# Kernel tuning notes

Measured on AMD Instinct MI355X. Metric: run time of the kernel, lower is better.

The kernel has to match this reference:

```python
import jax, jax.numpy as jnp
import numpy as np

B, H, L, T, V = 256, 512, 3, 200, 100  # batch, hidden, lstm layers, decode steps (text_max_len-1), vocab


def setup_inputs() -> dict:
    key = jax.random.key(0)
    ks = jax.random.split(key, 12)
    s = 0.04  # ~1/sqrt(512), keeps gates in a sane range like trained weights
    return {
        "feat": jax.random.normal(ks[0], (B, H), jnp.float32),
        "visual_w": jax.random.normal(ks[1], (H, H), jnp.float32) * s,
        "visual_b": jax.random.normal(ks[2], (H,), jnp.float32) * s,
        "embed": jax.random.normal(ks[3], (V, H), jnp.float32),
        "w_ih": jax.random.normal(ks[4], (L, 4 * H, H), jnp.float32) * s,
        "w_hh": jax.random.normal(ks[5], (L, 4 * H, H), jnp.float32) * s,
        "b_ih": jax.random.normal(ks[6], (L, 4 * H), jnp.float32) * s,
        "b_hh": jax.random.normal(ks[7], (L, 4 * H), jnp.float32) * s,
        "proj_w1": jax.random.normal(ks[8], (2 * H, H), jnp.float32) * s,
        "proj_b1": jax.random.normal(ks[9], (2 * H,), jnp.float32) * s,
        "proj_w2": jax.random.normal(ks[10], (V, 2 * H), jnp.float32) * s,
        "proj_b2": jax.random.normal(ks[11], (V,), jnp.float32) * s,
        "start_idx": 1,  # tokenizer.char2idx[sos_token]
    }


def _lstm_stack_step(h, c, x, w_ih, w_hh, b_ih, b_hh):
    # h, c: [L, B, H]; x: [B, H]. PyTorch gate order: i, f, g, o.
    hs, cs = [], []
    for l in range(L):
        gates = x @ w_ih[l].T + b_ih[l] + h[l] @ w_hh[l].T + b_hh[l]  # [B, 4H]
        i, f, g, o = jnp.split(gates, 4, axis=-1)
        c_new = jax.nn.sigmoid(f) * c[l] + jax.nn.sigmoid(i) * jnp.tanh(g)
        h_new = jax.nn.sigmoid(o) * jnp.tanh(c_new)
        hs.append(h_new)
        cs.append(c_new)
        x = h_new  # inter-layer dropout is identity in eval mode
    return jnp.stack(hs), jnp.stack(cs), x


def reference(feat, visual_w, visual_b, embed, w_ih, w_hh, b_ih, b_hh,
              proj_w1, proj_b1, proj_w2, proj_b2, start_idx):
    # encoder feature -> visual_proj (applied once in forward, once more in _init_hidden)
    feat1 = feat @ visual_w.T + visual_b
    h0_layer = feat1 @ visual_w.T + visual_b           # same weights for every layer
    h0 = jnp.broadcast_to(h0_layer, (L, B, H))
    c0 = jnp.zeros((L, B, H), jnp.float32)
    x0 = jnp.broadcast_to(embed[start_idx], (B, H))    # embedded <sos>

    def step(carry, _):
        h, c, x = carry
        h, c, top = _lstm_stack_step(h, c, x, w_ih, w_hh, b_ih, b_hh)
        # next input is the top-layer output, detached (inp = out[-1:].detach())
        return (h, c, jax.lax.stop_gradient(top)), top

    (_, _, _), outs = jax.lax.scan(step, (h0, c0, x0), None, length=T)  # outs: [T, B, H]
    res = outs.transpose(1, 0, 2)                                       # [B, T, H]
    hmid = jax.nn.gelu(res @ proj_w1.T + proj_b1, approximate=False)    # [B, T, 2H]
    logits = hmid @ proj_w2.T + proj_b2                                  # [B, T, V]
    return logits.transpose(0, 2, 1)                                     # [B, V, T]
```

## Files before the change

### kernel.cpp

```cpp
#include <hip/hip_runtime.h>
#include <hip/hip_bf16.h>
#include <hip/hip_fp16.h>

#define NB 256
#define NH 512
#define NL 3
#define NT 200
#define NV 100
#define NVP 112
#define NG 2048
#define NK 1024
#define NS (NT * NL)

using f16x8 = __attribute__((ext_vector_type(8))) _Float16;
using f32x4 = __attribute__((ext_vector_type(4))) float;
using u32x4 = __attribute__((ext_vector_type(4))) unsigned int;

__device__ __forceinline__ float sigf(float x) { return 1.f / (1.f + __expf(-x)); }
__device__ __forceinline__ float tanhf_(float x) { return 2.f / (1.f + __expf(-2.f * x)) - 1.f; }

__global__ void k_probe(int* __restrict__ rowmap, int* __restrict__ colmap) {
  const int lane = threadIdx.x & 63;
  f16x8 a, b;
  const _Float16 idv = (_Float16)(float)(lane & 15);
  const _Float16 inv = (_Float16)(1.f / 32.f);
#pragma unroll
  for (int j = 0; j < 8; ++j) { a[j] = idv; b[j] = inv; }
  f32x4 d = {0.f, 0.f, 0.f, 0.f};
  d = __builtin_amdgcn_mfma_f32_16x16x32_f16(a, b, d, 0, 0, 0);
#pragma unroll
  for (int r = 0; r < 4; ++r) rowmap[lane * 4 + r] = (int)(d[r] + 0.5f);
#pragma unroll
  for (int j = 0; j < 8; ++j) { a[j] = inv; b[j] = idv; }
  f32x4 e = {0.f, 0.f, 0.f, 0.f};
  e = __builtin_amdgcn_mfma_f32_16x16x32_f16(a, b, e, 0, 0, 0);
#pragma unroll
  for (int r = 0; r < 4; ++r) colmap[lane * 4 + r] = (int)(e[r] + 0.5f);
}

__global__ void k_prep_w(const float* __restrict__ w_ih, const float* __restrict__ w_hh,
                         const float* __restrict__ b_ih, const float* __restrict__ b_hh,
                         _Float16* __restrict__ Wih, _Float16* __restrict__ Whh,
                         float* __restrict__ bias) {
  const int stride = gridDim.x * blockDim.x;
  const int tid0 = blockIdx.x * blockDim.x + threadIdx.x;
  for (int idx = tid0; idx < NL * NG * NH; idx += stride) {
    const int k = idx & (NH - 1);
    const int r = (idx >> 9) & (NG - 1);
    const int l = idx >> 20;
    const int hu = r >> 2, g = r & 3;
    const size_t soff = ((size_t)(l * NG + g * NH + hu)) * NH + k;
    Wih[idx] = (_Float16)w_ih[soff];
    Whh[idx] = (_Float16)w_hh[soff];
  }
  for (int idx = tid0; idx < NL * NG; idx += stride) {
    const int r = idx & (NG - 1);
    const int l = idx >> 11;
    const int hu = r >> 2, g = r & 3;
    const int srow = l * NG + g * NH + hu;
    bias[idx] = b_ih[srow] + b_hh[srow];
  }
}

__global__ void k_prep_misc(const float* __restrict__ embed, const int* __restrict__ start_idx,
                            const float* __restrict__ w1, const float* __restrict__ b1,
                            const float* __restrict__ w2, const float* __restrict__ b2,
                            _Float16* __restrict__ x0, _Float16* __restrict__ pw1, float* __restrict__ pb1,
                            _Float16* __restrict__ pw2, float* __restrict__ pb2, int* __restrict__ flags) {
  const int stride = gridDim.x * blockDim.x;
  const int tid0 = blockIdx.x * blockDim.x + threadIdx.x;
  for (int i = tid0; i < 256 * 16; i += stride) flags[i] = 0;
  const int st = start_idx[0];
  for (int i = tid0; i < NB * NH; i += stride)
    x0[i] = (_Float16)embed[(size_t)st * NH + (i & (NH - 1))];
  for (int i = tid0; i < 2 * NH * NH; i += stride)
    pw1[i] = (_Float16)w1[i];
  for (int i = tid0; i < NVP * NK; i += stride) {
    const int r = i >> 10;
    pw2[i] = (_Float16)((r < NV) ? w2[i] : 0.f);
  }
  for (int i = tid0; i < 2 * NH; i += stride) pb1[i] = b1[i];
  for (int i = tid0; i < NVP; i += stride) pb2[i] = (i < NV) ? b2[i] : 0.f;
}

__global__ void k_gemv512(const float* __restrict__ x, const float* __restrict__ w,
                          const float* __restrict__ bias, float* __restrict__ out) {
  const int b = blockIdx.x;
  __shared__ float xs[NH];
  for (int i = threadIdx.x; i < NH; i += 256) xs[i] = x[(size_t)b * NH + i];
  __syncthreads();
  const int wave = threadIdx.x >> 6, lane = threadIdx.x & 63;
  for (int j = wave; j < NH; j += 4) {
    const float* wr = w + (size_t)j * NH;
    float s = 0.f;
#pragma unroll
    for (int i = 0; i < 8; ++i) s += wr[lane + i * 64] * xs[lane + i * 64];
#pragma unroll
    for (int o = 32; o > 0; o >>= 1) s += __shfl_down(s, o);
    if (lane == 0) out[(size_t)b * NH + j] = s + bias[j];
  }
}

__global__ void k_gemv2_h0(const float* __restrict__ feat1, const float* __restrict__ w,
                           const float* __restrict__ bias, _Float16* __restrict__ h0b) {
  const int b = blockIdx.x;
  __shared__ float xs[NH];
  for (int i = threadIdx.x; i < NH; i += 256) xs[i] = feat1[(size_t)b * NH + i];
  __syncthreads();
  const int wave = threadIdx.x >> 6, lane = threadIdx.x & 63;
  for (int j = wave; j < NH; j += 4) {
    const float* wr = w + (size_t)j * NH;
    float s = 0.f;
#pragma unroll
    for (int i = 0; i < 8; ++i) s += wr[lane + i * 64] * xs[lane + i * 64];
#pragma unroll
    for (int o = 32; o > 0; o >>= 1) s += __shfl_down(s, o);
    if (lane == 0) h0b[(size_t)b * NH + j] = (_Float16)(s + bias[j]);
  }
}

__global__ __launch_bounds__(512, 2) void k_lstm(const _Float16* __restrict__ Wih,
                                                 const _Float16* __restrict__ Whh,
                                                 const float* __restrict__ bias,
                                                 _Float16* hx, const _Float16* __restrict__ h0b,
                                                 const _Float16* __restrict__ x0,
                                                 _Float16* __restrict__ outs,
                                                 const int* __restrict__ rowmap,
                                                 const int* __restrict__ colmap,
                                                 int* flags) {
  const int tid = threadIdx.x;
  const int lane = tid & 63;
  const int wave = tid >> 6;
  const int bid = blockIdx.x;
  const int jj = bid & 31;
  const int bm = bid >> 5;
  const int bn = (jj & 7) * 4 + (jj >> 3);
  const int gbase = bm * 32;
  const int wn = wave & 3;
  const int kh = wave >> 2;
  const int lr = lane & 15;
  const int lh = lane >> 4;
  const int nb0 = bn * 64 + wn * 16;
  __shared__ _Float16 Als[32][512];
  __shared__ float gl[2][32][68];
  __shared__ float pend[3][2][32][68];
  __shared__ _Float16 hout[32][16];

  int rm[4], cm[4];
#pragma unroll
  for (int r = 0; r < 4; ++r) {
    rm[r] = rowmap[lane * 4 + r];
    cm[r] = colmap[lane * 4 + r];
  }
  const int bl_ = tid >> 4;
  const int hu = tid & 15;
  float creg[NL] = {0.f, 0.f, 0.f};
  float bsv[NL][4];
#pragma unroll
  for (int l = 0; l < NL; ++l)
#pragma unroll
    for (int g = 0; g < 4; ++g) bsv[l][g] = bias[l * NG + (bn * 16 + hu) * 4 + g];

  f16x8 wx[8], wh[8], areg[16];

#define PREFETCH(LX, LZ)                                                          \
  do {                                                                            \
    const _Float16* wbx = Wih + ((size_t)((LX) * NG + nb0 + lr)) * NH + kh * 256 + lh * 8; \
    const _Float16* wbh = Whh + ((size_t)((LZ) * NG + nb0 + lr)) * NH + kh * 256 + lh * 8; \
    _Pragma("unroll") for (int k_ = 0; k_ < 8; ++k_) {                            \
      wx[k_] = *(const f16x8*)(wbx + k_ * 32);                                    \
      wh[k_] = *(const f16x8*)(wbh + k_ * 32);                                    \
    }                                                                             \
  } while (0)

#define LOAD_AREG()                                                               \
  do {                                                                            \
    _Pragma("unroll") for (int kk = 0; kk < 8; ++kk) {                            \
      const int c_ = kh * 32 + kk * 4 + lh;                                       \
      areg[kk] = *(const f16x8*)&Als[lr][(c_ ^ (lr & 7)) * 8];                    \
      areg[8 + kk] = *(const f16x8*)&Als[16 + lr][(c_ ^ (lr & 7)) * 8];           \
    }                                                                             \
  } while (0)

#define STAGE_A(SRC, VOLQ)                                                        \
  do {                                                                            \
    _Pragma("unroll") for (int c = 0; c < 4; ++c) {                               \
      const int i_ = tid + c * 512;                                               \
      const int rr = i_ >> 6, cc = i_ & 63;                                       \
      u32x4 v_ = *(const VOLQ u32x4*)((SRC) + (size_t)(bm * 32 + rr) * NH + cc * 8); \
      *(u32x4*)&Als[rr][(cc ^ (rr & 7)) * 8] = v_;                                \
    }                                                                             \
  } while (0)

  STAGE_A(h0b, );
  __syncthreads();
  LOAD_AREG();
#pragma unroll 1
  for (int lp = 0; lp < 3; ++lp) {
    const _Float16* wbh = Whh + ((size_t)(lp * NG + nb0 + lr)) * NH + kh * 256 + lh * 8;
    f16x8 wt[8];
#pragma unroll
    for (int k_ = 0; k_ < 8; ++k_) wt[k_] = *(const f16x8*)(wbh + k_ * 32);
    f32x4 a0 = {0.f, 0.f, 0.f, 0.f}, a1 = {0.f, 0.f, 0.f, 0.f};
#pragma unroll
    for (int kk = 0; kk < 8; ++kk) {
      a0 = __builtin_amdgcn_mfma_f32_16x16x32_f16(areg[kk], wt[kk], a0, 0, 0, 0);
      a1 = __builtin_amdgcn_mfma_f32_16x16x32_f16(areg[8 + kk], wt[kk], a1, 0, 0, 0);
    }
#pragma unroll
    for (int r = 0; r < 4; ++r) {
      pend[lp][kh][rm[r]][wn * 16 + cm[r]] = a0[r];
      pend[lp][kh][16 + rm[r]][wn * 16 + cm[r]] = a1[r];
    }
  }
  PREFETCH(0, 2);
  __syncthreads();
  STAGE_A(x0, );
  __syncthreads();

#pragma unroll 1
  for (int t = 0; t < NT; ++t) {
#pragma unroll
    for (int l = 0; l < NL; ++l) {
      const int s = t * 3 + l;
      LOAD_AREG();
      {
        f32x4 a0 = {0.f, 0.f, 0.f, 0.f}, a1 = {0.f, 0.f, 0.f, 0.f};
#pragma unroll
        for (int kk = 0; kk < 8; ++kk) {
          a0 = __builtin_amdgcn_mfma_f32_16x16x32_f16(areg[kk], wx[kk], a0, 0, 0, 0);
          a1 = __builtin_amdgcn_mfma_f32_16x16x32_f16(areg[8 + kk], wx[kk], a1, 0, 0, 0);
        }
#pragma unroll
        for (int r = 0; r < 4; ++r) {
          gl[kh][rm[r]][wn * 16 + cm[r]] = a0[r];
          gl[kh][16 + rm[r]][wn * 16 + cm[r]] = a1[r];
        }
      }
      __syncthreads();
      {
        const f32x4 gx0 = *(const f32x4*)&gl[0][bl_][hu * 4];
        const f32x4 gx1 = *(const f32x4*)&gl[1][bl_][hu * 4];
        const f32x4 gh0 = *(const f32x4*)&pend[l][0][bl_][hu * 4];
        const f32x4 gh1 = *(const f32x4*)&pend[l][1][bl_][hu * 4];
        const float gi = gx0[0] + gx1[0] + gh0[0] + gh1[0] + bsv[l][0];
        const float gf = gx0[1] + gx1[1] + gh0[1] + gh1[1] + bsv[l][1];
        const float gg = gx0[2] + gx1[2] + gh0[2] + gh1[2] + bsv[l][2];
        const float go = gx0[3] + gx1[3] + gh0[3] + gh1[3] + bsv[l][3];
        const float cn = sigf(gf) * creg[l] + sigf(gi) * tanhf_(gg);
        const float hn = sigf(go) * tanhf_(cn);
        creg[l] = cn;
        hout[bl_][hu] = (_Float16)hn;
      }
      __syncthreads();
      if (wave == 0) {
        const int row = lane >> 1, half = lane & 1;
        _Float16* dst = hx + (size_t)(s & 1) * NB * NH + (size_t)(bm * 32 + row) * NH + bn * 16 + half * 8;
        u32x4 v = *(const u32x4*)&hout[row][half * 8];
        *(volatile u32x4*)dst = v;
      }
      if (s >= 1 && s <= NS - 3) {
        const int l2 = (l + 2) % 3;
        f32x4 a0 = {0.f, 0.f, 0.f, 0.f}, a1 = {0.f, 0.f, 0.f, 0.f};
#pragma unroll
        for (int kk = 0; kk < 8; ++kk) {
          a0 = __builtin_amdgcn_mfma_f32_16x16x32_f16(areg[kk], wh[kk], a0, 0, 0, 0);
          a1 = __builtin_amdgcn_mfma_f32_16x16x32_f16(areg[8 + kk], wh[kk], a1, 0, 0, 0);
        }
#pragma unroll
        for (int r = 0; r < 4; ++r) {
          pend[l2][kh][rm[r]][wn * 16 + cm[r]] = a0[r];
          pend[l2][kh][16 + rm[r]][wn * 16 + cm[r]] = a1[r];
        }
      }
      if (wave == 0) {
        asm volatile("s_waitcnt vmcnt(0)" ::: "memory");
        if (lane == 0) *(volatile int*)&flags[(gbase + jj) * 16] = s + 1;
      }
      if (wave == 1 && l == 2) {
        const int row = lane >> 1, half = lane & 1;
        _Float16* dst = outs + ((size_t)t * NB + bm * 32 + row) * NH + bn * 16 + half * 8;
        *(u32x4*)dst = *(const u32x4*)&hout[row][half * 8];
      }
      if (s < NS - 1) {
        PREFETCH((l + 1) % 3, l);
        if (lane < 32) {
          const volatile int* fp = (const volatile int*)&flags[(gbase + lane) * 16];
          while (*fp < s + 1) __builtin_amdgcn_s_sleep(1);
        }
        STAGE_A(hx + (size_t)(s & 1) * NB * NH, volatile);
        __syncthreads();
      }
    }
  }
#undef STAGE_A
#undef LOAD_AREG
#undef PREFETCH
}

__global__ __launch_bounds__(256) void k_proj(const _Float16* __restrict__ outs, const _Float16* __restrict__ pw1,
                                              const float* __restrict__ pb1, const _Float16* __restrict__ pw2,
                                              const float* __restrict__ pb2,
                                              const int* __restrict__ rowmap, const int* __restrict__ colmap,
                                              float* __restrict__ out) {
  const int tid = threadIdx.x;
  const int lane = tid & 63;
  const int wave = tid >> 6;
  const int lr = lane & 15;
  const int lh = lane >> 4;
  const int mbase = blockIdx.x * 16;
  __shared__ _Float16 hm[16][NK + 8];
  int rm[4], cm[4];
#pragma unroll
  for (int r = 0; r < 4; ++r) {
    rm[r] = rowmap[lane * 4 + r];
    cm[r] = colmap[lane * 4 + r];
  }
  const int mrow = mbase + lr;
  const _Float16* ap = outs + ((size_t)(mrow % NT) * NB + (mrow / NT)) * NH + lh * 8;
  for (int nf = 0; nf < 16; ++nf) {
    const int n0 = wave * 256 + nf * 16;
    f32x4 acc = {0.f, 0.f, 0.f, 0.f};
    const _Float16* bp = pw1 + (size_t)(n0 + lr) * NH + lh * 8;
#pragma unroll 4
    for (int kk = 0; kk < 16; ++kk) {
      f16x8 a = *(const f16x8*)(ap + kk * 32);
      f16x8 b = *(const f16x8*)(bp + kk * 32);
      acc = __builtin_amdgcn_mfma_f32_16x16x32_f16(a, b, acc, 0, 0, 0);
    }
#pragma unroll
    for (int r = 0; r < 4; ++r) {
      const float v = acc[r] + pb1[n0 + cm[r]];
      const float gv = 0.5f * v * (1.f + erff(v * 0.70710678118654752f));
      hm[rm[r]][n0 + cm[r]] = (_Float16)gv;
    }
  }
  __syncthreads();
  for (int nf = wave; nf < 7; nf += 4) {
    const int n0 = nf * 16;
    f32x4 acc = {0.f, 0.f, 0.f, 0.f};
    const _Float16* bp = pw2 + (size_t)(n0 + lr) * NK + lh * 8;
#pragma unroll 4
    for (int kk = 0; kk < 32; ++kk) {
      f16x8 a = *(const f16x8*)(&hm[lr][kk * 32 + lh * 8]);
      f16x8 b = *(const f16x8*)(bp + kk * 32);
      acc = __builtin_amdgcn_mfma_f32_16x16x32_f16(a, b, acc, 0, 0, 0);
    }
#pragma unroll
    for (int r = 0; r < 4; ++r) {
      const int v = n0 + cm[r];
      if (v < NV) {
        const int m = mbase + rm[r];
        out[((size_t)(m / NT) * NV + v) * NT + (m % NT)] = acc[r] + pb2[v];
      }
    }
  }
}

extern "C" void kernel_launch(void* const* d_in, const int* in_sizes, int n_in,
                              void* d_out, int out_size, void* d_ws, size_t ws_size,
                              hipStream_t stream) {
  const float* feat = (const float*)d_in[0];
  const float* visual_w = (const float*)d_in[1];
  const float* visual_b = (const float*)d_in[2];
  const float* embed = (const float*)d_in[3];
  const float* w_ih = (const float*)d_in[4];
  const float* w_hh = (const float*)d_in[5];
  const float* b_ih = (const float*)d_in[6];
  const float* b_hh = (const float*)d_in[7];
  const float* proj_w1 = (const float*)d_in[8];
  const float* proj_b1 = (const float*)d_in[9];
  const float* proj_w2 = (const float*)d_in[10];
  const float* proj_b2 = (const float*)d_in[11];
  const int* start_idx = (const int*)d_in[12];
  float* out = (float*)d_out;

  char* ws = (char*)d_ws;
  size_t off = 0;
  auto alloc = [&](size_t bytes) -> void* {
    void* p = ws + off;
    off += (bytes + 255) & ~(size_t)255;
    return p;
  };
  _Float16* Wih = (_Float16*)alloc((size_t)NL * NG * NH * 2);
  _Float16* Whh = (_Float16*)alloc((size_t)NL * NG * NH * 2);
  float* bias = (float*)alloc((size_t)NL * NG * 4);
  _Float16* hx = (_Float16*)alloc((size_t)2 * NB * NH * 2);
  _Float16* h0b = (_Float16*)alloc((size_t)NB * NH * 2);
  _Float16* x0 = (_Float16*)alloc((size_t)NB * NH * 2);
  _Float16* outsb = (_Float16*)alloc((size_t)NT * NB * NH * 2);
  float* feat1 = (float*)alloc((size_t)NB * NH * 4);
  _Float16* pw1 = (_Float16*)alloc((size_t)2 * NH * NH * 2);
  _Float16* pw2 = (_Float16*)alloc((size_t)NVP * NK * 2);
  float* pb1 = (float*)alloc((size_t)2 * NH * 4);
  float* pb2 = (float*)alloc((size_t)NVP * 4);
  int* flags = (int*)alloc(256 * 16 * 4);
  int* rowmap = (int*)alloc(256 * 4);
  int* colmap = (int*)alloc(256 * 4);
  if (off > ws_size) return;

  k_probe<<<dim3(1), dim3(64), 0, stream>>>(rowmap, colmap);
  k_prep_w<<<dim3(2048), dim3(256), 0, stream>>>(w_ih, w_hh, b_ih, b_hh, Wih, Whh, bias);
  k_prep_misc<<<dim3(1024), dim3(256), 0, stream>>>(embed, start_idx, proj_w1, proj_b1, proj_w2, proj_b2,
                                                    x0, pw1, pb1, pw2, pb2, flags);
  k_gemv512<<<dim3(NB), dim3(256), 0, stream>>>(feat, visual_w, visual_b, feat1);
  k_gemv2_h0<<<dim3(NB), dim3(256), 0, stream>>>(feat1, visual_w, visual_b, h0b);
  k_lstm<<<dim3(256), dim3(512), 0, stream>>>(Wih, Whh, bias, hx, h0b, x0, outsb, rowmap, colmap, flags);
  k_proj<<<dim3(3200), dim3(256), 0, stream>>>(outsb, pw1, pb1, pw2, pb2, rowmap, colmap, out);
}
```

Before: 4.791 ms.

## Repartition persistent LSTM blocks to 16-row batch groups with full-K waves

Each block of the persistent LSTM kernel now covers 16 batch rows and 128 gate columns, in groups of 16 blocks, instead of 32 rows and 64 columns in groups of 32 blocks. Each wave now does the full K=512 reduction itself, so the cross-wave partial-sum buffers and the extra LDS reads in the gate stage go away. This also shrinks each flag barrier from 32 blocks to 16, which should cut synchronisation latency on every step. The recurrent Whh weights are no longer prefetched into registers but loaded from global memory inside the MFMA loop, which may add load latency on the critical path; the host launch grid must also match the new mapping.

Result: slower. 8.648 ms (+80.5%).

```diff
diff --git a/kernel.cpp b/kernel.cpp
--- a/kernel.cpp
+++ b/kernel.cpp
@@ -132,19 +132,16 @@
   const int lane = tid & 63;
   const int wave = tid >> 6;
   const int bid = blockIdx.x;
-  const int jj = bid & 31;
-  const int bm = bid >> 5;
-  const int bn = (jj & 7) * 4 + (jj >> 3);
-  const int gbase = bm * 32;
-  const int wn = wave & 3;
-  const int kh = wave >> 2;
+  const int jj = bid & 15;
+  const int gm = bid >> 4;
+  const int gbase = gm * 16;
   const int lr = lane & 15;
   const int lh = lane >> 4;
-  const int nb0 = bn * 64 + wn * 16;
-  __shared__ _Float16 Als[32][512];
-  __shared__ float gl[2][32][68];
-  __shared__ float pend[3][2][32][68];
-  __shared__ _Float16 hout[32][16];
+  const int nb0 = jj * 128 + wave * 16;
+  __shared__ _Float16 Als[16][512];
+  __shared__ float gl[16][132];
+  __shared__ float pend[3][16][132];
+  __shared__ _Float16 hout[16][32];
 
   int rm[4], cm[4];
 #pragma unroll
@@ -152,42 +149,36 @@
     rm[r] = rowmap[lane * 4 + r];
     cm[r] = colmap[lane * 4 + r];
   }
-  const int bl_ = tid >> 4;
-  const int hu = tid & 15;
+  const int row_ = tid >> 5;
+  const int huL = tid & 31;
   float creg[NL] = {0.f, 0.f, 0.f};
   float bsv[NL][4];
 #pragma unroll
   for (int l = 0; l < NL; ++l)
 #pragma unroll
-    for (int g = 0; g < 4; ++g) bsv[l][g] = bias[l * NG + (bn * 16 + hu) * 4 + g];
-
-  f16x8 wx[8], wh[8], areg[16];
-
-#define PREFETCH(LX, LZ)                                                          \
+    for (int g = 0; g < 4; ++g) bsv[l][g] = bias[l * NG + (jj * 32 + huL) * 4 + g];
+
+  f16x8 wx[16], areg[16];
+
+#define PREFETCH(LX)                                                              \
   do {                                                                            \
-    const _Float16* wbx = Wih + ((size_t)((LX) * NG + nb0 + lr)) * NH + kh * 256 + lh * 8; \
-    const _Float16* wbh = Whh + ((size_t)((LZ) * NG + nb0 + lr)) * NH + kh * 256 + lh * 8; \
-    _Pragma("unroll") for (int k_ = 0; k_ < 8; ++k_) {                            \
-      wx[k_] = *(const f16x8*)(wbx + k_ * 32);                                    \
-      wh[k_] = *(const f16x8*)(wbh + k_ * 32);                                    \
-    }                                                                             \
+    const _Float16* wbx = Wih + ((size_t)((LX) * NG + nb0 + lr)) * NH + lh * 8;   \
+    _Pragma("unroll") for (int k_ = 0; k_ < 16; ++k_)                             \
+        wx[k_] = *(const f16x8*)(wbx + k_ * 32);                                  \
   } while (0)
 
 #define LOAD_AREG()                                                               \
   do {                                                                            \
-    _Pragma("unroll") for (int kk = 0; kk < 8; ++kk) {                            \
-      const int c_ = kh * 32 + kk * 4 + lh;                                       \
-      areg[kk] = *(const f16x8*)&Als[lr][(c_ ^ (lr & 7)) * 8];                    \
-      areg[8 + kk] = *(const f16x8*)&Als[16 + lr][(c_ ^ (lr & 7)) * 8];           \
-    }                                                                             \
+    _Pragma("unroll") for (int kk = 0; kk < 16; ++kk)                             \
+      areg[kk] = *(const f16x8*)&Als[lr][(((kk) * 4 + lh) ^ (lr & 7)) * 8];       \
   } while (0)
 
 #define STAGE_A(SRC, VOLQ)                                                        \
   do {                                                                            \
-    _Pragma("unroll") for (int c = 0; c < 4; ++c) {                               \
+    _Pragma("unroll") for (int c = 0; c < 2; ++c) {                               \
       const int i_ = tid + c * 512;                                               \
       const int rr = i_ >> 6, cc = i_ & 63;                                       \
-      u32x4 v_ = *(const VOLQ u32x4*)((SRC) + (size_t)(bm * 32 + rr) * NH + cc * 8); \
+      u32x4 v_ = *(const VOLQ u32x4*)((SRC) + (size_t)(gm * 16 + rr) * NH + cc * 8); \
       *(u32x4*)&Als[rr][(cc ^ (rr & 7)) * 8] = v_;                                \
     }                                                                             \
   } while (0)
@@ -197,23 +188,18 @@
   LOAD_AREG();
 #pragma unroll 1
   for (int lp = 0; lp < 3; ++lp) {
-    const _Float16* wbh = Whh + ((size_t)(lp * NG + nb0 + lr)) * NH + kh * 256 + lh * 8;
-    f16x8 wt[8];
-#pragma unroll
-    for (int k_ = 0; k_ < 8; ++k_) wt[k_] = *(const f16x8*)(wbh + k_ * 32);
-    f32x4 a0 = {0.f, 0.f, 0.f, 0.f}, a1 = {0.f, 0.f, 0.f, 0.f};
+    const _Float16* wbh = Whh + ((size_t)(lp * NG + nb0 + lr)) * NH + lh * 8;
+    f32x4 aA = {0.f, 0.f, 0.f, 0.f}, aB = {0.f, 0.f, 0.f, 0.f};
 #pragma unroll
     for (int kk = 0; kk < 8; ++kk) {
-      a0 = __builtin_amdgcn_mfma_f32_16x16x32_f16(areg[kk], wt[kk], a0, 0, 0, 0);
-      a1 = __builtin_amdgcn_mfma_f32_16x16x32_f16(areg[8 + kk], wt[kk], a1, 0, 0, 0);
-    }
-#pragma unroll
-    for (int r = 0; r < 4; ++r) {
-      pend[lp][kh][rm[r]][wn * 16 + cm[r]] = a0[r];
-      pend[lp][kh][16 + rm[r]][wn * 16 + cm[r]] = a1[r];
-    }
-  }
-  PREFETCH(0, 2);
+      aA = __builtin_amdgcn_mfma_f32_16x16x32_f16(areg[kk], *(const f16x8*)(wbh + kk * 32), aA, 0, 0, 0);
+      aB = __builtin_amdgcn_mfma_f32_16x16x32_f16(areg[8 + kk], *(const f16x8*)(wbh + (8 + kk) * 32), aB, 0, 0, 0);
+    }
+#pragma unroll
+    for (int r = 0; r < 4; ++r)
+      pend[lp][rm[r]][wave * 16 + cm[r]] = aA[r] + aB[r];
+  }
+  PREFETCH(0);
   __syncthreads();
   STAGE_A(x0, );
   __syncthreads();
@@ -225,66 +211,61 @@
       const int s = t * 3 + l;
       LOAD_AREG();
       {
-        f32x4 a0 = {0.f, 0.f, 0.f, 0.f}, a1 = {0.f, 0.f, 0.f, 0.f};
+        f32x4 aA = {0.f, 0.f, 0.f, 0.f}, aB = {0.f, 0.f, 0.f, 0.f};
 #pragma unroll
         for (int kk = 0; kk < 8; ++kk) {
-          a0 = __builtin_amdgcn_mfma_f32_16x16x32_f16(areg[kk], wx[kk], a0, 0, 0, 0);
-          a1 = __builtin_amdgcn_mfma_f32_16x16x32_f16(areg[8 + kk], wx[kk], a1, 0, 0, 0);
+          aA = __builtin_amdgcn_mfma_f32_16x16x32_f16(areg[kk], wx[kk], aA, 0, 0, 0);
+          aB = __builtin_amdgcn_mfma_f32_16x16x32_f16(areg[8 + kk], wx[8 + kk], aB, 0, 0, 0);
         }
 #pragma unroll
-        for (int r = 0; r < 4; ++r) {
-          gl[kh][rm[r]][wn * 16 + cm[r]] = a0[r];
-          gl[kh][16 + rm[r]][wn * 16 + cm[r]] = a1[r];
-        }
+        for (int r = 0; r < 4; ++r)
+          gl[rm[r]][wave * 16 + cm[r]] = aA[r] + aB[r];
       }
       __syncthreads();
       {
-        const f32x4 gx0 = *(const f32x4*)&gl[0][bl_][hu * 4];
-        const f32x4 gx1 = *(const f32x4*)&gl[1][bl_][hu * 4];
-        const f32x4 gh0 = *(const f32x4*)&pend[l][0][bl_][hu * 4];
-        const f32x4 gh1 = *(const f32x4*)&pend[l][1][bl_][hu * 4];
-        const float gi = gx0[0] + gx1[0] + gh0[0] + gh1[0] + bsv[l][0];
-        const float gf = gx0[1] + gx1[1] + gh0[1] + gh1[1] + bsv[l][1];
-        const float gg = gx0[2] + gx1[2] + gh0[2] + gh1[2] + bsv[l][2];
-        const float go = gx0[3] + gx1[3] + gh0[3] + gh1[3] + bsv[l][3];
+        const f32x4 gx = *(const f32x4*)&gl[row_][huL * 4];
+        const f32x4 gh = *(const f32x4*)&pend[l][row_][huL * 4];
+        const float gi = gx[0] + gh[0] + bsv[l][0];
+        const float gf = gx[1] + gh[1] + bsv[l][1];
+        const float gg = gx[2] + gh[2] + bsv[l][2];
+        const float go = gx[3] + gh[3] + bsv[l][3];
         const float cn = sigf(gf) * creg[l] + sigf(gi) * tanhf_(gg);
         const float hn = sigf(go) * tanhf_(cn);
         creg[l] = cn;
-        hout[bl_][hu] = (_Float16)hn;
+        hout[row_][huL] = (_Float16)hn;
       }
       __syncthreads();
       if (wave == 0) {
-        const int row = lane >> 1, half = lane & 1;
-        _Float16* dst = hx + (size_t)(s & 1) * NB * NH + (size_t)(bm * 32 + row) * NH + bn * 16 + half * 8;
-        u32x4 v = *(const u32x4*)&hout[row][half * 8];
+        const int row = lane >> 2, q = lane & 3;
+        _Float16* dst = hx + (size_t)(s & 1) * NB * NH + (size_t)(gm * 16 + row) * NH + jj * 32 + q * 8;
+        u32x4 v = *(const u32x4*)&hout[row][q * 8];
         *(volatile u32x4*)dst = v;
       }
       if (s >= 1 && s <= NS - 3) {
         const int l2 = (l + 2) % 3;
-        f32x4 a0 = {0.f, 0.f, 0.f, 0.f}, a1 = {0.f, 0.f, 0.f, 0.f};
+        const _Float16* wbh = Whh + ((size_t)(l2 * NG + nb0 + lr)) * NH + lh * 8;
+        f32x4 aA = {0.f, 0.f, 0.f, 0.f}, aB = {0.f, 0.f, 0.f, 0.f};
 #pragma unroll
         for (int kk = 0; kk < 8; ++kk) {
-          a0 = __builtin_amdgcn_mfma_f32_16x16x32_f16(areg[kk], wh[kk], a0, 0, 0, 0);
-          a1 = __builtin_amdgcn_mfma_f32_16x16x32_f16(areg[8 + kk], wh[kk], a1, 0, 0, 0);
+          aA = __builtin_amdgcn_mfma_f32_16x16x32_f16(areg[kk], *(const f16x8*)(wbh + kk * 32), aA, 0, 0, 0);
+          aB = __builtin_amdgcn_mfma_f32_16x16x32_f16(areg[8 + kk], *(const f16x8*)(wbh + (8 + kk) * 32), aB, 0, 0, 0);
         }
 #pragma unroll
-        for (int r = 0; r < 4; ++r) {
-          pend[l2][kh][rm[r]][wn * 16 + cm[r]] = a0[r];
-          pend[l2][kh][16 + rm[r]][wn * 16 + cm[r]] = a1[r];
-        }
+        for (int r = 0; r < 4; ++r)
+          pend[l2][rm[r]][wave * 16 + cm[r]] = aA[r] + aB[r];
       }
       if (wave == 0) {
         asm volatile("s_waitcnt vmcnt(0)" ::: "memory");
         if (lane == 0) *(volatile int*)&flags[(gbase + jj) * 16] = s + 1;
       }
       if (wave == 1 && l == 2) {
-        const int row = lane >> 1, half = lane & 1;
-        _Float16* dst = outs + ((size_t)t * NB + bm * 32 + row) * NH + bn * 16 + half * 8;
-        *(u32x4*)dst = *(const u32x4*)&hout[row][half * 8];
+        const int row = lane >> 2, q = lane & 3;
+        _Float16* dst = outs + ((size_t)t * NB + gm * 16 + row) * NH + jj * 32 + q * 8;
+        *(u32x4*)dst = *(const u32x4*)&hout[row][q * 8];
       }
       if (s < NS - 1) {
-        PREFETCH((l + 1) % 3, l);
-        if (lane < 32) {
+        PREFETCH((l + 1) % 3);
+        if (lane < 16) {
           const volatile int* fp = (const volatile int*)&flags[(gbase + lane) * 16];
           while (*fp < s + 1) __builtin_amdgcn_s_sleep(1);
         }
```

## Merge setup kernels and retile projection to 32-row blocks with register-held A

Applied to the files above, without the earlier changes.

Fuses the probe and two weight-preparation kernels into one setup launch, removing two kernel launches. The projection kernel now handles 32 output rows per block: each wave keeps its 16x512 activation slice in registers and loops over half of the hidden columns, using two independent MFMA accumulator chains. This halves the number of blocks and the repeated loads of the first projection weights, at the cost of more registers and more shared memory per block, which may lower occupancy.

New measurement: 4.578 ms. 4.5% less time.

```diff
diff --git a/kernel.cpp b/kernel.cpp
--- a/kernel.cpp
+++ b/kernel.cpp
@@ -19,31 +19,36 @@
 __device__ __forceinline__ float sigf(float x) { return 1.f / (1.f + __expf(-x)); }
 __device__ __forceinline__ float tanhf_(float x) { return 2.f / (1.f + __expf(-2.f * x)) - 1.f; }
 
-__global__ void k_probe(int* __restrict__ rowmap, int* __restrict__ colmap) {
-  const int lane = threadIdx.x & 63;
-  f16x8 a, b;
-  const _Float16 idv = (_Float16)(float)(lane & 15);
-  const _Float16 inv = (_Float16)(1.f / 32.f);
-#pragma unroll
-  for (int j = 0; j < 8; ++j) { a[j] = idv; b[j] = inv; }
-  f32x4 d = {0.f, 0.f, 0.f, 0.f};
-  d = __builtin_amdgcn_mfma_f32_16x16x32_f16(a, b, d, 0, 0, 0);
-#pragma unroll
-  for (int r = 0; r < 4; ++r) rowmap[lane * 4 + r] = (int)(d[r] + 0.5f);
-#pragma unroll
-  for (int j = 0; j < 8; ++j) { a[j] = inv; b[j] = idv; }
-  f32x4 e = {0.f, 0.f, 0.f, 0.f};
-  e = __builtin_amdgcn_mfma_f32_16x16x32_f16(a, b, e, 0, 0, 0);
-#pragma unroll
-  for (int r = 0; r < 4; ++r) colmap[lane * 4 + r] = (int)(e[r] + 0.5f);
-}
-
-__global__ void k_prep_w(const float* __restrict__ w_ih, const float* __restrict__ w_hh,
-                         const float* __restrict__ b_ih, const float* __restrict__ b_hh,
-                         _Float16* __restrict__ Wih, _Float16* __restrict__ Whh,
-                         float* __restrict__ bias) {
+__global__ void k_setup(const float* __restrict__ w_ih, const float* __restrict__ w_hh,
+                        const float* __restrict__ b_ih, const float* __restrict__ b_hh,
+                        const float* __restrict__ embed, const int* __restrict__ start_idx,
+                        const float* __restrict__ w1, const float* __restrict__ b1,
+                        const float* __restrict__ w2, const float* __restrict__ b2,
+                        _Float16* __restrict__ Wih, _Float16* __restrict__ Whh,
+                        float* __restrict__ bias, _Float16* __restrict__ x0,
+                        _Float16* __restrict__ pw1, float* __restrict__ pb1,
+                        _Float16* __restrict__ pw2, float* __restrict__ pb2,
+                        int* __restrict__ flags, int* __restrict__ rowmap, int* __restrict__ colmap) {
   const int stride = gridDim.x * blockDim.x;
   const int tid0 = blockIdx.x * blockDim.x + threadIdx.x;
+  if (blockIdx.x == 0 && threadIdx.x < 64) {
+    const int lane = threadIdx.x & 63;
+    f16x8 a, b;
+    const _Float16 idv = (_Float16)(float)(lane & 15);
+    const _Float16 inv = (_Float16)(1.f / 32.f);
+#pragma unroll
+    for (int j = 0; j < 8; ++j) { a[j] = idv; b[j] = inv; }
+    f32x4 d = {0.f, 0.f, 0.f, 0.f};
+    d = __builtin_amdgcn_mfma_f32_16x16x32_f16(a, b, d, 0, 0, 0);
+#pragma unroll
+    for (int r = 0; r < 4; ++r) rowmap[lane * 4 + r] = (int)(d[r] + 0.5f);
+#pragma unroll
+    for (int j = 0; j < 8; ++j) { a[j] = inv; b[j] = idv; }
+    f32x4 e = {0.f, 0.f, 0.f, 0.f};
+    e = __builtin_amdgcn_mfma_f32_16x16x32_f16(a, b, e, 0, 0, 0);
+#pragma unroll
+    for (int r = 0; r < 4; ++r) colmap[lane * 4 + r] = (int)(e[r] + 0.5f);
+  }
   for (int idx = tid0; idx < NL * NG * NH; idx += stride) {
     const int k = idx & (NH - 1);
     const int r = (idx >> 9) & (NG - 1);
@@ -60,15 +65,6 @@
     const int srow = l * NG + g * NH + hu;
     bias[idx] = b_ih[srow] + b_hh[srow];
   }
-}
-
-__global__ void k_prep_misc(const float* __restrict__ embed, const int* __restrict__ start_idx,
-                            const float* __restrict__ w1, const float* __restrict__ b1,
-                            const float* __restrict__ w2, const float* __restrict__ b2,
-                            _Float16* __restrict__ x0, _Float16* __restrict__ pw1, float* __restrict__ pb1,
-                            _Float16* __restrict__ pw2, float* __restrict__ pb2, int* __restrict__ flags) {
-  const int stride = gridDim.x * blockDim.x;
-  const int tid0 = blockIdx.x * blockDim.x + threadIdx.x;
   for (int i = tid0; i < 256 * 16; i += stride) flags[i] = 0;
   const int st = start_idx[0];
   for (int i = tid0; i < NB * NH; i += stride)
@@ -308,41 +304,47 @@
   const int wave = tid >> 6;
   const int lr = lane & 15;
   const int lh = lane >> 4;
-  const int mbase = blockIdx.x * 16;
-  __shared__ _Float16 hm[16][NK + 8];
+  const int mbase = blockIdx.x * 32;
+  const int mt_w = wave >> 1;
+  const int nh_w = wave & 1;
+  __shared__ _Float16 hm[32][NK + 8];
   int rm[4], cm[4];
 #pragma unroll
   for (int r = 0; r < 4; ++r) {
     rm[r] = rowmap[lane * 4 + r];
     cm[r] = colmap[lane * 4 + r];
   }
-  const int mrow = mbase + lr;
+  const int mrow = mbase + mt_w * 16 + lr;
   const _Float16* ap = outs + ((size_t)(mrow % NT) * NB + (mrow / NT)) * NH + lh * 8;
-  for (int nf = 0; nf < 16; ++nf) {
-    const int n0 = wave * 256 + nf * 16;
-    f32x4 acc = {0.f, 0.f, 0.f, 0.f};
+  f16x8 areg[16];
+#pragma unroll
+  for (int kk = 0; kk < 16; ++kk) areg[kk] = *(const f16x8*)(ap + kk * 32);
+#pragma unroll 1
+  for (int nf = 0; nf < 32; ++nf) {
+    const int n0 = nh_w * 512 + nf * 16;
     const _Float16* bp = pw1 + (size_t)(n0 + lr) * NH + lh * 8;
-#pragma unroll 4
-    for (int kk = 0; kk < 16; ++kk) {
-      f16x8 a = *(const f16x8*)(ap + kk * 32);
-      f16x8 b = *(const f16x8*)(bp + kk * 32);
-      acc = __builtin_amdgcn_mfma_f32_16x16x32_f16(a, b, acc, 0, 0, 0);
+    f32x4 aA = {0.f, 0.f, 0.f, 0.f}, aB = {0.f, 0.f, 0.f, 0.f};
+#pragma unroll
+    for (int kk = 0; kk < 8; ++kk) {
+      aA = __builtin_amdgcn_mfma_f32_16x16x32_f16(areg[kk], *(const f16x8*)(bp + kk * 32), aA, 0, 0, 0);
+      aB = __builtin_amdgcn_mfma_f32_16x16x32_f16(areg[8 + kk], *(const f16x8*)(bp + (8 + kk) * 32), aB, 0, 0, 0);
     }
 #pragma unroll
     for (int r = 0; r < 4; ++r) {
-      const float v = acc[r] + pb1[n0 + cm[r]];
+      const float v = aA[r] + aB[r] + pb1[n0 + cm[r]];
       const float gv = 0.5f * v * (1.f + erff(v * 0.70710678118654752f));
-      hm[rm[r]][n0 + cm[r]] = (_Float16)gv;
-    }
-  }
-  __syncthreads();
-  for (int nf = wave; nf < 7; nf += 4) {
+      hm[mt_w * 16 + rm[r]][n0 + cm[r]] = (_Float16)gv;
+    }
+  }
+  __syncthreads();
+  for (int unit = wave; unit < 14; unit += 4) {
+    const int mt = unit / 7, nf = unit % 7;
     const int n0 = nf * 16;
     f32x4 acc = {0.f, 0.f, 0.f, 0.f};
     const _Float16* bp = pw2 + (size_t)(n0 + lr) * NK + lh * 8;
 #pragma unroll 4
     for (int kk = 0; kk < 32; ++kk) {
-      f16x8 a = *(const f16x8*)(&hm[lr][kk * 32 + lh * 8]);
+      f16x8 a = *(const f16x8*)(&hm[mt * 16 + lr][kk * 32 + lh * 8]);
       f16x8 b = *(const f16x8*)(bp + kk * 32);
       acc = __builtin_amdgcn_mfma_f32_16x16x32_f16(a, b, acc, 0, 0, 0);
     }
@@ -350,7 +352,7 @@
     for (int r = 0; r < 4; ++r) {
       const int v = n0 + cm[r];
       if (v < NV) {
-        const int m = mbase + rm[r];
+        const int m = mbase + mt * 16 + rm[r];
         out[((size_t)(m / NT) * NV + v) * NT + (m % NT)] = acc[r] + pb2[v];
       }
     }
@@ -399,12 +401,12 @@
   int* colmap = (int*)alloc(256 * 4);
   if (off > ws_size) return;
 
-  k_probe<<<dim3(1), dim3(64), 0, stream>>>(rowmap, colmap);
-  k_prep_w<<<dim3(2048), dim3(256), 0, stream>>>(w_ih, w_hh, b_ih, b_hh, Wih, Whh, bias);
-  k_prep_misc<<<dim3(1024), dim3(256), 0, stream>>>(embed, start_idx, proj_w1, proj_b1, proj_w2, proj_b2,
-                                                    x0, pw1, pb1, pw2, pb2, flags);
+  k_setup<<<dim3(2048), dim3(256), 0, stream>>>(w_ih, w_hh, b_ih, b_hh, embed, start_idx,
+                                                proj_w1, proj_b1, proj_w2, proj_b2,
+                                                Wih, Whh, bias, x0, pw1, pb1, pw2, pb2,
+                                                flags, rowmap, colmap);
   k_gemv512<<<dim3(NB), dim3(256), 0, stream>>>(feat, visual_w, visual_b, feat1);
   k_gemv2_h0<<<dim3(NB), dim3(256), 0, stream>>>(feat1, visual_w, visual_b, h0b);
   k_lstm<<<dim3(256), dim3(512), 0, stream>>>(Wih, Whh, bias, hx, h0b, x0, outsb, rowmap, colmap, flags);
-  k_proj<<<dim3(3200), dim3(256), 0, stream>>>(outsb, pw1, pb1, pw2, pb2, rowmap, colmap, out);
-}
+  k_proj<<<dim3(1600), dim3(256), 0, stream>>>(outsb, pw1, pb1, pw2, pb2, rowmap, colmap, out);
+}
```
